# Performance work log

Measured on AMD Instinct MI355X. Metric: run time of the kernel, lower is better.

Reference implementation:

```python
import jax, jax.numpy as jnp
import numpy as np

B, S, H, L = 16, 128, 512, 43  # batch, seq_len, bilstm_output_size, dep_label_size
NEG = -10000.0


def setup_inputs() -> dict:
    key = jax.random.key(0)
    ks = jax.random.split(key, 7)
    sentence_repr = jax.random.normal(ks[0], (B, S, H), dtype=jnp.float32)
    labels = jax.random.normal(ks[1], (B, S, L), dtype=jnp.float32)
    heads = jax.random.randint(ks[2], (B, S), 0, S)
    words = jax.random.randint(ks[3], (B, S), 0, 30000)
    sent_id = jnp.arange(B, dtype=jnp.int32).reshape(B, 1)
    scale = 1.0 / np.sqrt(H + L).astype(np.float32)
    u_w = jax.random.normal(ks[4], (H + L, H), dtype=jnp.float32) * scale  # u_a kernel
    u_b = jnp.zeros((H,), dtype=jnp.float32)                               # u_a bias
    w_w = jax.random.normal(ks[5], (H + L, H), dtype=jnp.float32) * scale  # w_a kernel
    w_b = jnp.zeros((H,), dtype=jnp.float32)                               # w_a bias
    v_w = jax.random.normal(ks[6], (H, 1), dtype=jnp.float32) * (1.0 / np.sqrt(H).astype(np.float32))  # v_a_inv, no bias
    return {"sentence_repr": sentence_repr, "labels": labels, "heads": heads,
            "words": words, "sent_id": sent_id,
            "u_w": u_w, "u_b": u_b, "w_w": w_w, "w_b": w_b, "v_w": v_w}


def reference(sentence_repr, labels, heads, words, sent_id, u_w, u_b, w_w, w_b, v_w):
    b, s, h = sentence_repr.shape
    # u_a(concat(sentence_repr, zeros[..,43])) == sentence_repr @ u_w[:h] + u_b
    # (the label slots multiply zeros, exactly as the original tf.concat with tf.zeros)
    u = sentence_repr @ u_w[:h] + u_b                      # [B,S,H]
    dep = jnp.concatenate([sentence_repr, labels], axis=-1)  # [B,S,H+L]
    w = dep @ w_w + w_b                                    # [B,S,H]
    # vectorized version of the per-token loop:
    # scores[b,i,j] = v_a_inv . tanh(u_a(repr_j) + w_a(dependant_i))
    scores = jnp.squeeze(jnp.tanh(u[:, None, :, :] + w[:, :, None, :]) @ v_w, -1)  # [B,S,S]
    # head_mask: position j == i gets -10000
    diag = jnp.eye(s, dtype=bool)
    scores = jnp.where(diag[None, :, :], NEG, scores)
    # pad mask over candidate heads j (applied since batch_size > 1)
    pad_mask = (words == 0)                                # [B,S]
    scores = jnp.where(pad_mask[:, None, :], NEG, scores)
    # loss = sum over i=1..S-1 of mean-over-batch sparse CE from logits
    logp = jax.nn.log_softmax(scores, axis=-1)             # [B,S,S]
    ce = -jnp.take_along_axis(logp, heads[..., None], axis=-1)[..., 0]  # [B,S]
    loss = jnp.sum(jnp.mean(ce[:, 1:], axis=0))
    # parent_prob_dict values: exp(head_probs) per dependant token i=1..S-1
    probs = jnp.exp(scores[:, 1:, :])                      # [B,S-1,S]
    return loss, probs
```

## Files before the change

### kernel.cpp

```cpp
#include <hip/hip_runtime.h>
#include <hip/hip_bf16.h>
#include <math.h>

#define BB 16
#define SS 128
#define HH 512
#define LL 43
#define NEGV -10000.0f
#define M_TOT (BB*SS)
#define KP 576

#define LOG2E 1.44269504088896f
#define TWO_LOG2E 2.88539008177793f
#define LN2 0.69314718055995f

typedef __bf16 bf16_t;
typedef __attribute__((ext_vector_type(8)))  __bf16 bf16x8;
typedef __attribute__((ext_vector_type(16))) float  f32x16;

__device__ __forceinline__ float fast_exp2(float x) { return __builtin_amdgcn_exp2f(x); }
__device__ __forceinline__ float fast_rcp(float x)  { return __builtin_amdgcn_rcpf(x); }
__device__ __forceinline__ float fast_log2(float x) { return __builtin_amdgcn_logf(x); }
__device__ __forceinline__ float exp_fast(float x)  { return fast_exp2(x * LOG2E); }

__device__ __forceinline__ float tanh_pre(float xp) {
    float e = fast_exp2(xp);
    return fmaf(-2.0f, fast_rcp(e + 1.0f), 1.0f);
}

__global__ __launch_bounds__(256)
void split_kernel(const float* __restrict__ repr, const float* __restrict__ labels,
                  const float* __restrict__ u_w, const float* __restrict__ w_w,
                  bf16_t* __restrict__ Ah, bf16_t* __restrict__ Al,
                  bf16_t* __restrict__ Buh, bf16_t* __restrict__ Bul,
                  bf16_t* __restrict__ Bwh, bf16_t* __restrict__ Bwl) {
    const int tid = threadIdx.x;
    if (blockIdx.x < 288) {
        const int kt = blockIdx.x >> 4;
        const int nt = blockIdx.x & 15;
        const int k0 = kt * 32, n0 = nt * 32;
        __shared__ float tu[32][33], tw[32][33];
        {
            const int r  = tid >> 3;
            const int c4 = (tid & 7) << 2;
            const int k  = k0 + r;
            float4 fu = make_float4(0.f, 0.f, 0.f, 0.f);
            float4 fw = make_float4(0.f, 0.f, 0.f, 0.f);
            if (k < HH)      fu = *(const float4*)&u_w[(size_t)k * HH + n0 + c4];
            if (k < HH + LL) fw = *(const float4*)&w_w[(size_t)k * HH + n0 + c4];
            tu[r][c4+0] = fu.x; tu[r][c4+1] = fu.y; tu[r][c4+2] = fu.z; tu[r][c4+3] = fu.w;
            tw[r][c4+0] = fw.x; tw[r][c4+1] = fw.y; tw[r][c4+2] = fw.z; tw[r][c4+3] = fw.w;
        }
        __syncthreads();
        {
            const int nr = tid >> 3;
            const int k4 = (tid & 7) << 2;
            union { bf16_t h[4]; uint2 v; } uh, ul, wh, wl;
#pragma unroll
            for (int q = 0; q < 4; ++q) {
                float xu = tu[k4 + q][nr];
                float xw = tw[k4 + q][nr];
                bf16_t hu = (bf16_t)xu; bf16_t lu = (bf16_t)(xu - (float)hu);
                bf16_t hw = (bf16_t)xw; bf16_t lw = (bf16_t)(xw - (float)hw);
                uh.h[q] = hu; ul.h[q] = lu; wh.h[q] = hw; wl.h[q] = lw;
            }
            const size_t o = (size_t)(n0 + nr) * KP + k0 + k4;
            *(uint2*)&Buh[o] = uh.v;  *(uint2*)&Bul[o] = ul.v;
            *(uint2*)&Bwh[o] = wh.v;  *(uint2*)&Bwl[o] = wl.v;
        }
    } else {
        const int chunk = (blockIdx.x - 288) * 256 + tid;
        const int m  = chunk / 144;
        const int c4 = chunk - m * 144;
        const int k  = c4 << 2;
        float x[4];
        if (k <= HH - 4) {
            float4 f = *(const float4*)&repr[(size_t)m * HH + k];
            x[0] = f.x; x[1] = f.y; x[2] = f.z; x[3] = f.w;
        } else {
#pragma unroll
            for (int q = 0; q < 4; ++q) {
                const int kk = k + q;
                x[q] = (kk < HH + LL) ? labels[(size_t)m * LL + (kk - HH)] : 0.f;
            }
        }
        union { bf16_t h[4]; uint2 v; } ph, pl;
#pragma unroll
        for (int q = 0; q < 4; ++q) {
            bf16_t hi = (bf16_t)x[q];
            ph.h[q] = hi;
            pl.h[q] = (bf16_t)(x[q] - (float)hi);
        }
        const size_t o = (size_t)m * KP + k;
        *(uint2*)&Ah[o] = ph.v;
        *(uint2*)&Al[o] = pl.v;
    }
}

__global__ __launch_bounds__(256)
void gemm_mfma(const bf16_t* __restrict__ Ah, const bf16_t* __restrict__ Al,
               const bf16_t* __restrict__ Buh, const bf16_t* __restrict__ Bul,
               const bf16_t* __restrict__ Bwh, const bf16_t* __restrict__ Bwl,
               const float* __restrict__ u_b, const float* __restrict__ w_b,
               float* __restrict__ u_out, float* __restrict__ w_out) {
    __shared__ bf16_t sm[6][64][40];

    const int tid  = threadIdx.x;
    const int bm   = blockIdx.x & 31;
    const int bn   = blockIdx.x >> 5;
    const int m0   = bm * 64, n0 = bn * 64;
    const int wv   = tid >> 6, lane = tid & 63;
    const int wm   = wv >> 1, wn = wv & 1;
    const int ln31 = lane & 31, g = lane >> 5;

    const int sr = tid >> 2;
    const int sc = tid & 3;

    f32x16 accu = {0,0,0,0,0,0,0,0,0,0,0,0,0,0,0,0};
    f32x16 accw = {0,0,0,0,0,0,0,0,0,0,0,0,0,0,0,0};

    const size_t aoff = (size_t)(m0 + sr) * KP;
    const size_t boff = (size_t)(n0 + sr) * KP;

    for (int kt = 0; kt < KP / 32; ++kt) {
        const int kc = kt * 32 + sc * 8;
        *(uint4*)&sm[0][sr][sc * 8] = *(const uint4*)&Ah [aoff + kc];
        *(uint4*)&sm[1][sr][sc * 8] = *(const uint4*)&Al [aoff + kc];
        *(uint4*)&sm[2][sr][sc * 8] = *(const uint4*)&Buh[boff + kc];
        *(uint4*)&sm[3][sr][sc * 8] = *(const uint4*)&Bul[boff + kc];
        *(uint4*)&sm[4][sr][sc * 8] = *(const uint4*)&Bwh[boff + kc];
        *(uint4*)&sm[5][sr][sc * 8] = *(const uint4*)&Bwl[boff + kc];
        __syncthreads();

#pragma unroll
        for (int ks = 0; ks < 2; ++ks) {
            const int co = ks * 16 + g * 8;
            bf16x8 a_h = *(const bf16x8*)&sm[0][wm * 32 + ln31][co];
            bf16x8 a_l = *(const bf16x8*)&sm[1][wm * 32 + ln31][co];
            bf16x8 buh = *(const bf16x8*)&sm[2][wn * 32 + ln31][co];
            bf16x8 bul = *(const bf16x8*)&sm[3][wn * 32 + ln31][co];
            bf16x8 bwh = *(const bf16x8*)&sm[4][wn * 32 + ln31][co];
            bf16x8 bwl = *(const bf16x8*)&sm[5][wn * 32 + ln31][co];
            accu = __builtin_amdgcn_mfma_f32_32x32x16_bf16(a_h, buh, accu, 0, 0, 0);
            accu = __builtin_amdgcn_mfma_f32_32x32x16_bf16(a_h, bul, accu, 0, 0, 0);
            accu = __builtin_amdgcn_mfma_f32_32x32x16_bf16(a_l, buh, accu, 0, 0, 0);
            accw = __builtin_amdgcn_mfma_f32_32x32x16_bf16(a_h, bwh, accw, 0, 0, 0);
            accw = __builtin_amdgcn_mfma_f32_32x32x16_bf16(a_h, bwl, accw, 0, 0, 0);
            accw = __builtin_amdgcn_mfma_f32_32x32x16_bf16(a_l, bwh, accw, 0, 0, 0);
        }
        __syncthreads();
    }

    const int C = n0 + wn * 32 + ln31;
    const float ub = u_b[C], wb = w_b[C];
#pragma unroll
    for (int rg = 0; rg < 16; ++rg) {
        const int m = (rg & 3) + 8 * (rg >> 2) + 4 * g;
        const int R = m0 + wm * 32 + m;
        u_out[(size_t)R * HH + C] = (accu[rg] + ub) * TWO_LOG2E;
        w_out[(size_t)R * HH + C] = (accw[rg] + wb) * TWO_LOG2E;
    }
}

__global__ __launch_bounds__(256)
void scores_v2(const float* __restrict__ u, const float* __restrict__ w,
               const float* __restrict__ v_w, const int* __restrict__ heads,
               const int* __restrict__ words,
               float* __restrict__ out,
               float* __restrict__ ce_out) {
    const int blk = blockIdx.x;
    const int r   = blk & 7;
    const int q   = blk >> 3;
    const int b   = r * 2 + (q & 1);
    const int i0  = (q >> 1) * 4;

    const int tid  = threadIdx.x;
    const int wv   = tid >> 6;
    const int lane = tid & 63;
    const int ig   = wv >> 1;
    const int jh   = wv & 1;
    const int j    = jh * 64 + lane;
    const int ia   = i0 + ig * 2;

    const float* __restrict__ up  = &u[(size_t)(b * SS + j) * HH];
    const float* __restrict__ w0p = &w[(size_t)(b * SS + ia) * HH];
    const float* __restrict__ w1p = w0p + HH;

    float acc0 = 0.f, acc1 = 0.f;
#pragma unroll 2
    for (int h = 0; h < HH; h += 8) {
        float4 ua = *(const float4*)&up[h];
        float4 ub = *(const float4*)&up[h + 4];
        float4 va = *(const float4*)&v_w[h];
        float4 vb = *(const float4*)&v_w[h + 4];
        float4 w0a = *(const float4*)&w0p[h];
        float4 w0b = *(const float4*)&w0p[h + 4];
        float4 w1a = *(const float4*)&w1p[h];
        float4 w1b = *(const float4*)&w1p[h + 4];
#define STEP(UU, VV, W0, W1)                                  \
        acc0 = fmaf(VV, tanh_pre(UU + W0), acc0);             \
        acc1 = fmaf(VV, tanh_pre(UU + W1), acc1);
        STEP(ua.x, va.x, w0a.x, w1a.x)
        STEP(ua.y, va.y, w0a.y, w1a.y)
        STEP(ua.z, va.z, w0a.z, w1a.z)
        STEP(ua.w, va.w, w0a.w, w1a.w)
        STEP(ub.x, vb.x, w0b.x, w1b.x)
        STEP(ub.y, vb.y, w0b.y, w1b.y)
        STEP(ub.z, vb.z, w0b.z, w1b.z)
        STEP(ub.w, vb.w, w0b.w, w1b.w)
#undef STEP
    }

    const bool colpad = (words[b * SS + j] == 0);
    float s0 = (colpad || j == ia)     ? NEGV : acc0;
    float s1 = (colpad || j == ia + 1) ? NEGV : acc1;

    __shared__ float s_lds[4][SS];
    s_lds[ig * 2 + 0][j] = s0;
    s_lds[ig * 2 + 1][j] = s1;

    if (ia >= 1)
        out[1 + (size_t)(b * (SS - 1) + (ia - 1)) * SS + j] = exp_fast(s0);
    out[1 + (size_t)(b * (SS - 1) + ia) * SS + j] = exp_fast(s1);

    __syncthreads();

    const int i  = i0 + wv;
    float t0 = s_lds[wv][lane];
    float t1 = s_lds[wv][lane + 64];
    float m = fmaxf(t0, t1);
#pragma unroll
    for (int off = 32; off > 0; off >>= 1) m = fmaxf(m, __shfl_xor(m, off));
    float e = exp_fast(t0 - m) + exp_fast(t1 - m);
#pragma unroll
    for (int off = 32; off > 0; off >>= 1) e += __shfl_xor(e, off);

    const int hd = heads[b * SS + i];
    const float sh = s_lds[wv][hd];
    const float ce = m + fast_log2(e) * LN2 - sh;
    if (lane == 0) ce_out[b * SS + i] = (i >= 1) ? ce : 0.f;
}

__global__ __launch_bounds__(256)
void loss_sum(const float* __restrict__ ce, float* __restrict__ out) {
    __shared__ double sd[256];
    const int tid = threadIdx.x;
    double s = 0.0;
    for (int k = tid; k < M_TOT; k += 256) s += (double)ce[k];
    sd[tid] = s;
    __syncthreads();
    for (int off = 128; off > 0; off >>= 1) {
        if (tid < off) sd[tid] += sd[tid + off];
        __syncthreads();
    }
    if (tid == 0) out[0] = (float)(sd[0] * (1.0 / (double)BB));
}

extern "C" void kernel_launch(void* const* d_in, const int* in_sizes, int n_in,
                              void* d_out, int out_size, void* d_ws, size_t ws_size,
                              hipStream_t stream) {
    const float* repr   = (const float*)d_in[0];
    const float* labels = (const float*)d_in[1];
    const int*   heads  = (const int*)d_in[2];
    const int*   words  = (const int*)d_in[3];
    const float* u_w    = (const float*)d_in[5];
    const float* u_b    = (const float*)d_in[6];
    const float* w_w    = (const float*)d_in[7];
    const float* w_b    = (const float*)d_in[8];
    const float* v_w    = (const float*)d_in[9];

    float* out = (float*)d_out;

    char* ws = (char*)d_ws;
    size_t cur = 0;
    float*  u_ws = (float*)(ws + cur);  cur += (size_t)M_TOT * HH * 4;
    float*  w_ws = (float*)(ws + cur);  cur += (size_t)M_TOT * HH * 4;
    bf16_t* Ah   = (bf16_t*)(ws + cur); cur += (size_t)M_TOT * KP * 2;
    bf16_t* Al   = (bf16_t*)(ws + cur); cur += (size_t)M_TOT * KP * 2;
    bf16_t* Buh  = (bf16_t*)(ws + cur); cur += (size_t)HH * KP * 2;
    bf16_t* Bul  = (bf16_t*)(ws + cur); cur += (size_t)HH * KP * 2;
    bf16_t* Bwh  = (bf16_t*)(ws + cur); cur += (size_t)HH * KP * 2;
    bf16_t* Bwl  = (bf16_t*)(ws + cur); cur += (size_t)HH * KP * 2;
    float*  ce_ws = (float*)(ws + cur);

    split_kernel<<<dim3(1440), dim3(256), 0, stream>>>(
        repr, labels, u_w, w_w, Ah, Al, Buh, Bul, Bwh, Bwl);
    gemm_mfma<<<dim3(256), dim3(256), 0, stream>>>(
        Ah, Al, Buh, Bul, Bwh, Bwl, u_b, w_b, u_ws, w_ws);
    scores_v2<<<dim3(512), dim3(256), 0, stream>>>(
        u_ws, w_ws, v_w, heads, words, out, ce_ws);
    loss_sum<<<dim3(1), dim3(256), 0, stream>>>(ce_ws, out);
}
```

Before: 147.0 us.

## Factor tanh constant out via v-sum and stage w/v rows in LDS

The scores kernel now computes sum v*1/(1+e^x) and recovers sum v*tanh as vsum - 2*acc, which drops one FMA per element from the hot tanh loop. The w rows and v vector are staged in shared memory, and each thread now handles one dependant row instead of two. This doubles the grid to 1024 blocks and halves per-thread work. In exchange, the u row is now loaded by twice as many blocks, which adds global traffic, and there is a small precision change from the algebraic rearrangement.

```diff
diff --git a/kernel.cpp b/kernel.cpp
--- a/kernel.cpp
+++ b/kernel.cpp
@@ -22,11 +22,6 @@
 __device__ __forceinline__ float fast_rcp(float x)  { return __builtin_amdgcn_rcpf(x); }
 __device__ __forceinline__ float fast_log2(float x) { return __builtin_amdgcn_logf(x); }
 __device__ __forceinline__ float exp_fast(float x)  { return fast_exp2(x * LOG2E); }
-
-__device__ __forceinline__ float tanh_pre(float xp) {
-    float e = fast_exp2(xp);
-    return fmaf(-2.0f, fast_rcp(e + 1.0f), 1.0f);
-}
 
 __global__ __launch_bounds__(256)
 void split_kernel(const float* __restrict__ repr, const float* __restrict__ labels,
@@ -163,82 +158,97 @@
 }
 
 __global__ __launch_bounds__(256)
-void scores_v2(const float* __restrict__ u, const float* __restrict__ w,
+void scores_v3(const float* __restrict__ u, const float* __restrict__ w,
                const float* __restrict__ v_w, const int* __restrict__ heads,
                const int* __restrict__ words,
                float* __restrict__ out,
                float* __restrict__ ce_out) {
     const int blk = blockIdx.x;
-    const int r   = blk & 7;
-    const int q   = blk >> 3;
-    const int b   = r * 2 + (q & 1);
-    const int i0  = (q >> 1) * 4;
+    const int b   = (blk & 7) * 2 + ((blk >> 3) & 1);
+    const int i0  = (blk >> 4) * 2;
 
     const int tid  = threadIdx.x;
     const int wv   = tid >> 6;
     const int lane = tid & 63;
-    const int ig   = wv >> 1;
+    const int ir   = wv >> 1;
     const int jh   = wv & 1;
+    const int i    = i0 + ir;
     const int j    = jh * 64 + lane;
-    const int ia   = i0 + ig * 2;
-
-    const float* __restrict__ up  = &u[(size_t)(b * SS + j) * HH];
-    const float* __restrict__ w0p = &w[(size_t)(b * SS + ia) * HH];
-    const float* __restrict__ w1p = w0p + HH;
-
-    float acc0 = 0.f, acc1 = 0.f;
+
+    __shared__ float sw[2][HH];
+    __shared__ float sv[HH];
+    __shared__ float s_sc[2][SS];
+    __shared__ float s_vsum;
+
+    for (int c = tid; c < 384; c += 256) {
+        const int seg = c >> 7;
+        const int off = (c & 127) << 2;
+        const float* src = (seg == 0) ? &w[(size_t)(b * SS + i0) * HH + off]
+                         : (seg == 1) ? &w[(size_t)(b * SS + i0 + 1) * HH + off]
+                                      : &v_w[off];
+        float* dst = (seg == 0) ? &sw[0][off] : (seg == 1) ? &sw[1][off] : &sv[off];
+        *(float4*)dst = *(const float4*)src;
+    }
+    __syncthreads();
+
+    if (wv == 0) {
+        float vs = 0.f;
+#pragma unroll
+        for (int q = 0; q < 8; ++q) vs += sv[lane * 8 + q];
+#pragma unroll
+        for (int off = 32; off > 0; off >>= 1) vs += __shfl_xor(vs, off);
+        if (lane == 0) s_vsum = vs;
+    }
+
+    const float* __restrict__ up = &u[(size_t)(b * SS + j) * HH];
+    float acc = 0.f;
 #pragma unroll 2
     for (int h = 0; h < HH; h += 8) {
         float4 ua = *(const float4*)&up[h];
         float4 ub = *(const float4*)&up[h + 4];
-        float4 va = *(const float4*)&v_w[h];
-        float4 vb = *(const float4*)&v_w[h + 4];
-        float4 w0a = *(const float4*)&w0p[h];
-        float4 w0b = *(const float4*)&w0p[h + 4];
-        float4 w1a = *(const float4*)&w1p[h];
-        float4 w1b = *(const float4*)&w1p[h + 4];
-#define STEP(UU, VV, W0, W1)                                  \
-        acc0 = fmaf(VV, tanh_pre(UU + W0), acc0);             \
-        acc1 = fmaf(VV, tanh_pre(UU + W1), acc1);
-        STEP(ua.x, va.x, w0a.x, w1a.x)
-        STEP(ua.y, va.y, w0a.y, w1a.y)
-        STEP(ua.z, va.z, w0a.z, w1a.z)
-        STEP(ua.w, va.w, w0a.w, w1a.w)
-        STEP(ub.x, vb.x, w0b.x, w1b.x)
-        STEP(ub.y, vb.y, w0b.y, w1b.y)
-        STEP(ub.z, vb.z, w0b.z, w1b.z)
-        STEP(ub.w, vb.w, w0b.w, w1b.w)
+        float4 va = *(const float4*)&sv[h];
+        float4 vb = *(const float4*)&sv[h + 4];
+        float4 wa = *(const float4*)&sw[ir][h];
+        float4 wb = *(const float4*)&sw[ir][h + 4];
+#define STEP(UU, VV, WW)                                          \
+        acc = fmaf(VV, fast_rcp(fast_exp2(UU + WW) + 1.0f), acc);
+        STEP(ua.x, va.x, wa.x)
+        STEP(ua.y, va.y, wa.y)
+        STEP(ua.z, va.z, wa.z)
+        STEP(ua.w, va.w, wa.w)
+        STEP(ub.x, vb.x, wb.x)
+        STEP(ub.y, vb.y, wb.y)
+        STEP(ub.z, vb.z, wb.z)
+        STEP(ub.w, vb.w, wb.w)
 #undef STEP
     }
-
+    __syncthreads();
+
+    const float vsum = s_vsum;
+    float s = fmaf(-2.0f, acc, vsum);
     const bool colpad = (words[b * SS + j] == 0);
-    float s0 = (colpad || j == ia)     ? NEGV : acc0;
-    float s1 = (colpad || j == ia + 1) ? NEGV : acc1;
-
-    __shared__ float s_lds[4][SS];
-    s_lds[ig * 2 + 0][j] = s0;
-    s_lds[ig * 2 + 1][j] = s1;
-
-    if (ia >= 1)
-        out[1 + (size_t)(b * (SS - 1) + (ia - 1)) * SS + j] = exp_fast(s0);
-    out[1 + (size_t)(b * (SS - 1) + ia) * SS + j] = exp_fast(s1);
-
+    if (colpad || j == i) s = NEGV;
+
+    s_sc[ir][j] = s;
+    if (i >= 1)
+        out[1 + (size_t)(b * (SS - 1) + (i - 1)) * SS + j] = exp_fast(s);
     __syncthreads();
 
-    const int i  = i0 + wv;
-    float t0 = s_lds[wv][lane];
-    float t1 = s_lds[wv][lane + 64];
-    float m = fmaxf(t0, t1);
-#pragma unroll
-    for (int off = 32; off > 0; off >>= 1) m = fmaxf(m, __shfl_xor(m, off));
-    float e = exp_fast(t0 - m) + exp_fast(t1 - m);
-#pragma unroll
-    for (int off = 32; off > 0; off >>= 1) e += __shfl_xor(e, off);
-
-    const int hd = heads[b * SS + i];
-    const float sh = s_lds[wv][hd];
-    const float ce = m + fast_log2(e) * LN2 - sh;
-    if (lane == 0) ce_out[b * SS + i] = (i >= 1) ? ce : 0.f;
+    if (jh == 0) {
+        float t0 = s_sc[ir][lane];
+        float t1 = s_sc[ir][lane + 64];
+        float m = fmaxf(t0, t1);
+#pragma unroll
+        for (int off = 32; off > 0; off >>= 1) m = fmaxf(m, __shfl_xor(m, off));
+        float e = exp_fast(t0 - m) + exp_fast(t1 - m);
+#pragma unroll
+        for (int off = 32; off > 0; off >>= 1) e += __shfl_xor(e, off);
+
+        const int hd = heads[b * SS + i];
+        const float sh = s_sc[ir][hd];
+        const float ce = m + fast_log2(e) * LN2 - sh;
+        if (lane == 0) ce_out[b * SS + i] = (i >= 1) ? ce : 0.f;
+    }
 }
 
 __global__ __launch_bounds__(256)
@@ -287,7 +297,7 @@
         repr, labels, u_w, w_w, Ah, Al, Buh, Bul, Bwh, Bwl);
     gemm_mfma<<<dim3(256), dim3(256), 0, stream>>>(
         Ah, Al, Buh, Bul, Bwh, Bwl, u_b, w_b, u_ws, w_ws);
-    scores_v2<<<dim3(512), dim3(256), 0, stream>>>(
+    scores_v3<<<dim3(1024), dim3(256), 0, stream>>>(
         u_ws, w_ws, v_w, heads, words, out, ce_ws);
     loss_sum<<<dim3(1), dim3(256), 0, stream>>>(ce_ws, out);
 }
```

New measurement: 163.5 us. +11.3%, slower.

## Hoist tanh affine term out of scores loop and split H across waves

Applied to the files above, without the earlier changes.

The scores kernel now uses tanh(x)=1-2/(e^{2x}+1), so the constant 1 term becomes a precomputed sum of v and only v·rcp(exp2+1) is accumulated per element. This saves one FMA per tanh. Work is also re-partitioned: each block handles 2 dependants instead of 4, with the hidden dimension split in half across wave pairs and the partials combined through LDS. The grid doubles to 1024 blocks for more parallelism, at the cost of extra LDS traffic, two block barriers, and waves left idle in the epilogue.

```diff
diff --git a/kernel.cpp b/kernel.cpp
--- a/kernel.cpp
+++ b/kernel.cpp
@@ -22,11 +22,6 @@
 __device__ __forceinline__ float fast_rcp(float x)  { return __builtin_amdgcn_rcpf(x); }
 __device__ __forceinline__ float fast_log2(float x) { return __builtin_amdgcn_logf(x); }
 __device__ __forceinline__ float exp_fast(float x)  { return fast_exp2(x * LOG2E); }
-
-__device__ __forceinline__ float tanh_pre(float xp) {
-    float e = fast_exp2(xp);
-    return fmaf(-2.0f, fast_rcp(e + 1.0f), 1.0f);
-}
 
 __global__ __launch_bounds__(256)
 void split_kernel(const float* __restrict__ repr, const float* __restrict__ labels,
@@ -163,43 +158,55 @@
 }
 
 __global__ __launch_bounds__(256)
-void scores_v2(const float* __restrict__ u, const float* __restrict__ w,
+void scores_v5(const float* __restrict__ u, const float* __restrict__ w,
                const float* __restrict__ v_w, const int* __restrict__ heads,
                const int* __restrict__ words,
                float* __restrict__ out,
                float* __restrict__ ce_out) {
     const int blk = blockIdx.x;
-    const int r   = blk & 7;
-    const int q   = blk >> 3;
-    const int b   = r * 2 + (q & 1);
-    const int i0  = (q >> 1) * 4;
+    const int b   = (blk & 7) * 2 + ((blk >> 3) & 1);
+    const int i0  = (blk >> 4) * 2;
 
     const int tid  = threadIdx.x;
     const int wv   = tid >> 6;
     const int lane = tid & 63;
-    const int ig   = wv >> 1;
+    const int hh   = wv >> 1;
     const int jh   = wv & 1;
     const int j    = jh * 64 + lane;
-    const int ia   = i0 + ig * 2;
-
-    const float* __restrict__ up  = &u[(size_t)(b * SS + j) * HH];
-    const float* __restrict__ w0p = &w[(size_t)(b * SS + ia) * HH];
+    const int h0   = hh * (HH / 2);
+
+    __shared__ float part[2][2][SS];
+    __shared__ float s_sc[2][SS];
+    __shared__ float s_vsum;
+
+    if (wv == 0) {
+        float4 a = *(const float4*)&v_w[lane * 8];
+        float4 c = *(const float4*)&v_w[lane * 8 + 4];
+        float vs = a.x + a.y + a.z + a.w + c.x + c.y + c.z + c.w;
+#pragma unroll
+        for (int off = 32; off > 0; off >>= 1) vs += __shfl_xor(vs, off);
+        if (lane == 0) s_vsum = vs;
+    }
+
+    const float* __restrict__ up  = &u[(size_t)(b * SS + j) * HH + h0];
+    const float* __restrict__ w0p = &w[(size_t)(b * SS + i0) * HH + h0];
     const float* __restrict__ w1p = w0p + HH;
+    const float* __restrict__ vp  = &v_w[h0];
 
     float acc0 = 0.f, acc1 = 0.f;
 #pragma unroll 2
-    for (int h = 0; h < HH; h += 8) {
-        float4 ua = *(const float4*)&up[h];
-        float4 ub = *(const float4*)&up[h + 4];
-        float4 va = *(const float4*)&v_w[h];
-        float4 vb = *(const float4*)&v_w[h + 4];
+    for (int h = 0; h < HH / 2; h += 8) {
+        float4 ua  = *(const float4*)&up[h];
+        float4 ub  = *(const float4*)&up[h + 4];
+        float4 va  = *(const float4*)&vp[h];
+        float4 vb  = *(const float4*)&vp[h + 4];
         float4 w0a = *(const float4*)&w0p[h];
         float4 w0b = *(const float4*)&w0p[h + 4];
         float4 w1a = *(const float4*)&w1p[h];
         float4 w1b = *(const float4*)&w1p[h + 4];
-#define STEP(UU, VV, W0, W1)                                  \
-        acc0 = fmaf(VV, tanh_pre(UU + W0), acc0);             \
-        acc1 = fmaf(VV, tanh_pre(UU + W1), acc1);
+#define STEP(UU, VV, W0, W1)                                          \
+        acc0 = fmaf(VV, fast_rcp(fast_exp2(UU + W0) + 1.0f), acc0);   \
+        acc1 = fmaf(VV, fast_rcp(fast_exp2(UU + W1) + 1.0f), acc1);
         STEP(ua.x, va.x, w0a.x, w1a.x)
         STEP(ua.y, va.y, w0a.y, w1a.y)
         STEP(ua.z, va.z, w0a.z, w1a.z)
@@ -210,35 +217,42 @@
         STEP(ub.w, vb.w, w0b.w, w1b.w)
 #undef STEP
     }
-
-    const bool colpad = (words[b * SS + j] == 0);
-    float s0 = (colpad || j == ia)     ? NEGV : acc0;
-    float s1 = (colpad || j == ia + 1) ? NEGV : acc1;
-
-    __shared__ float s_lds[4][SS];
-    s_lds[ig * 2 + 0][j] = s0;
-    s_lds[ig * 2 + 1][j] = s1;
-
-    if (ia >= 1)
-        out[1 + (size_t)(b * (SS - 1) + (ia - 1)) * SS + j] = exp_fast(s0);
-    out[1 + (size_t)(b * (SS - 1) + ia) * SS + j] = exp_fast(s1);
-
+    part[hh][0][j] = acc0;
+    part[hh][1][j] = acc1;
     __syncthreads();
 
-    const int i  = i0 + wv;
-    float t0 = s_lds[wv][lane];
-    float t1 = s_lds[wv][lane + 64];
-    float m = fmaxf(t0, t1);
-#pragma unroll
-    for (int off = 32; off > 0; off >>= 1) m = fmaxf(m, __shfl_xor(m, off));
-    float e = exp_fast(t0 - m) + exp_fast(t1 - m);
-#pragma unroll
-    for (int off = 32; off > 0; off >>= 1) e += __shfl_xor(e, off);
-
-    const int hd = heads[b * SS + i];
-    const float sh = s_lds[wv][hd];
-    const float ce = m + fast_log2(e) * LN2 - sh;
-    if (lane == 0) ce_out[b * SS + i] = (i >= 1) ? ce : 0.f;
+    if (hh == 0) {
+        const float vsum = s_vsum;
+        const bool colpad = (words[b * SS + j] == 0);
+#pragma unroll
+        for (int r = 0; r < 2; ++r) {
+            const int i = i0 + r;
+            float s = fmaf(-2.0f, part[0][r][j] + part[1][r][j], vsum);
+            if (colpad || j == i) s = NEGV;
+            s_sc[r][j] = s;
+            if (i >= 1)
+                out[1 + (size_t)(b * (SS - 1) + (i - 1)) * SS + j] = exp_fast(s);
+        }
+    }
+    __syncthreads();
+
+    if (hh == 1) {
+        const int r = jh;
+        const int i = i0 + r;
+        float t0 = s_sc[r][lane];
+        float t1 = s_sc[r][lane + 64];
+        float m = fmaxf(t0, t1);
+#pragma unroll
+        for (int off = 32; off > 0; off >>= 1) m = fmaxf(m, __shfl_xor(m, off));
+        float e = exp_fast(t0 - m) + exp_fast(t1 - m);
+#pragma unroll
+        for (int off = 32; off > 0; off >>= 1) e += __shfl_xor(e, off);
+
+        const int hd = heads[b * SS + i];
+        const float sh = s_sc[r][hd];
+        const float ce = m + fast_log2(e) * LN2 - sh;
+        if (lane == 0) ce_out[b * SS + i] = (i >= 1) ? ce : 0.f;
+    }
 }
 
 __global__ __launch_bounds__(256)
@@ -287,7 +301,7 @@
         repr, labels, u_w, w_w, Ah, Al, Buh, Bul, Bwh, Bwl);
     gemm_mfma<<<dim3(256), dim3(256), 0, stream>>>(
         Ah, Al, Buh, Bul, Bwh, Bwl, u_b, w_b, u_ws, w_ws);
-    scores_v2<<<dim3(512), dim3(256), 0, stream>>>(
+    scores_v5<<<dim3(1024), dim3(256), 0, stream>>>(
         u_ws, w_ws, v_w, heads, words, out, ce_ws);
     loss_sum<<<dim3(1), dim3(256), 0, stream>>>(ce_ws, out);
 }
```

Result: slower. 155.6 us (+5.9%).
